# Kernel tuning notes

Hardware: AMD Instinct MI355X
Metric: run time of the kernel (lower is better)

## Reference

```python
import jax, jax.numpy as jnp
import numpy as np

L, B, D = 512, 16, 256
H = 4            # MAX_DIFF == num_heads
MAX_BONDS = 6
MAX_DIFF = 4
PROB_SHIFT = 0.3


def _attn_weights(x, Wqk, Wq, bq, Wk, bk, mask):
    """Per-head softmax(QK^T/sqrt(hd)) with key padding mask.
    x: [b,l,d]; Wqk: [d,2d] (the inc/dec_qk pre-projection);
    Wq/Wk: [d,d] (MHA in_proj, stored x@W layout); mask: [b,l] bool (True=masked).
    Returns [b,h,l,l]. The V path / out_proj of the torch MHA are discarded
    by the original module, so they are omitted here.
    """
    b, l, d = x.shape
    hd = d // H
    q = x @ Wqk[:, :d]
    k = x @ Wqk[:, d:]
    Q = (q @ Wq + bq).reshape(b, l, H, hd)
    K = (k @ Wk + bk).reshape(b, l, H, hd)
    scores = jnp.einsum('blhd,bmhd->bhlm', Q, K) / np.sqrt(hd)
    scores = jnp.where(mask[:, None, None, :], -jnp.inf, scores)
    return jax.nn.softmax(scores, axis=-1)


def setup_inputs() -> dict:
    key = jax.random.key(0)
    ks = jax.random.split(key, 16)
    s = 0.05
    p = lambda k, shape: jax.random.normal(k, shape, jnp.float32) * s
    # key_padding_mask: last 64 positions padded (True == masked)
    src_mask = jnp.broadcast_to(jnp.arange(L)[None, :] >= (L - 64), (B, L))
    return {
        'molecule_embedding': jax.random.normal(ks[0], (L, B, D), jnp.float32),
        'src_bond': jax.random.randint(ks[1], (B, L, MAX_BONDS), 0, L, jnp.int32),
        'src_mask': src_mask,
        'W_inc_qk': p(ks[2], (D, 2 * D)),
        'Wq_inc': p(ks[3], (D, D)), 'bq_inc': p(ks[4], (D,)),
        'Wk_inc': p(ks[5], (D, D)), 'bk_inc': p(ks[6], (D,)),
        'W_dec_qk': p(ks[7], (D, 2 * D)),
        'Wq_dec': p(ks[8], (D, D)), 'bq_dec': p(ks[9], (D,)),
        'Wk_dec': p(ks[10], (D, D)), 'bk_dec': p(ks[11], (D,)),
        'Wc': p(ks[12], (MAX_DIFF, MAX_DIFF)), 'bc': p(ks[13], (MAX_DIFF,)),
    }


def reference(molecule_embedding, src_bond, src_mask,
              W_inc_qk, Wq_inc, bq_inc, Wk_inc, bk_inc,
              W_dec_qk, Wq_dec, bq_dec, Wk_dec, bk_dec,
              Wc, bc):
    x = jnp.transpose(molecule_embedding, (1, 0, 2))  # [b,l,d]
    b, l, _ = x.shape

    inc = _attn_weights(x, W_inc_qk, Wq_inc, bq_inc, Wk_inc, bk_inc, src_mask)
    dec = _attn_weights(x, W_dec_qk, Wq_dec, bq_dec, Wk_dec, bk_dec, src_mask)

    pad = (~src_mask).astype(jnp.float32)              # 1 - mask
    pm2 = pad[:, :, None] * pad[:, None, :]            # [b,l,l]

    # cls_layer((inc-dec).permute(0,2,3,1)) * (MAX_DIFF*pad_mask)[...,None]
    diff = (jnp.einsum('bhlm,hc->blmc', inc - dec, Wc) + bc)
    diff = diff * (MAX_DIFF * pm2)[..., None]          # [b,l,l,4]

    # src_bond has last dim == MAX_BONDS -> one-hot neighbor counts
    src_w = jax.nn.one_hot(src_bond, l, dtype=jnp.float32).sum(axis=2) * pm2  # [b,l,l]
    eye = jnp.eye(l, dtype=jnp.float32)
    src_w = src_w * (1.0 - eye)[None]                  # zero diagonal

    # _shift_probs(src_weight.long(), prob_shift, MAX_DIFF)
    oh = jax.nn.one_hot(src_w.astype(jnp.int32), MAX_DIFF, dtype=jnp.float32)
    probs = oh * (1.0 - PROB_SHIFT) + (1.0 - oh) * (PROB_SHIFT / (MAX_DIFF - 1))
    probs = probs / probs.sum(axis=-1, keepdims=True)

    return jnp.log(probs + 1e-6) + diff                # [b,l,l,4]
```

## Files before the change

kernel.cpp:

```cpp
#include <hip/hip_runtime.h>
#include <stdint.h>

typedef unsigned short u16t;
typedef short s8v __attribute__((ext_vector_type(8)));
typedef float f4v __attribute__((ext_vector_type(4)));

#define MFMA16 __builtin_amdgcn_mfma_f32_16x16x32_bf16
#define QKN (16*4*512*64)

__device__ __forceinline__ u16t f2bf(float f) {
  unsigned u = __builtin_bit_cast(unsigned, f);
  u += 0x7fffu + ((u >> 16) & 1u);
  return (u16t)(u >> 16);
}

__global__ __launch_bounds__(256) void prep_kernel(
    const float* __restrict__ Wiqk, const float* __restrict__ Wqi, const float* __restrict__ Wki,
    const float* __restrict__ Wdqk, const float* __restrict__ Wqd, const float* __restrict__ Wkd,
    u16t* __restrict__ weffT, const int* __restrict__ mraw, int* __restrict__ mdst) {
  __shared__ float At[16][65];
  __shared__ float Bt[16][65];
  __shared__ int mode;
  const int tid = threadIdx.x;

  if (blockIdx.z == 4) {
    if (tid == 0) mode = 0;
    __syncthreads();
    unsigned v0 = (unsigned)mraw[tid], v1 = (unsigned)mraw[tid + 256];
    if (v0 == 0x3F800000u || v1 == 0x3F800000u) mode = 2;
    __syncthreads();
    if (mode == 0 && (v0 > 1u || v1 > 1u)) mode = 1;
    __syncthreads();
    const int g = blockIdx.y * 4 + blockIdx.x;
#pragma unroll
    for (int i = 0; i < 2; ++i) {
      int idx = g * 512 + i * 256 + tid;
      int m;
      if (mode == 2)      m = (((const float*)mraw)[idx] != 0.0f) ? 1 : 0;
      else if (mode == 1) m = ((const unsigned char*)mraw)[idx];
      else                m = mraw[idx];
      mdst[idx] = m;
    }
    return;
  }

  const int n0 = blockIdx.x * 64;
  const int d0 = blockIdx.y * 64;
  const int p  = blockIdx.z;
  const float* A2  = (p == 0) ? Wqi : (p == 1) ? Wki : (p == 2) ? Wqd : Wkd;
  const float* Wqk = (p < 2) ? Wiqk : Wdqk;
  const int aoff = (p & 1) * 256;
  const int tx = tid & 15, ty = tid >> 4;

  float acc[4][4];
#pragma unroll
  for (int i = 0; i < 4; ++i)
#pragma unroll
    for (int j = 0; j < 4; ++j) acc[i][j] = 0.f;

  for (int k0 = 0; k0 < 256; k0 += 16) {
    __syncthreads();
    {
      int nn = tid & 63, kr = tid >> 6;
#pragma unroll
      for (int pass = 0; pass < 4; ++pass) {
        int kk = kr + pass * 4;
        At[kk][nn] = A2[(size_t)(k0 + kk) * 256 + n0 + nn];
      }
      int kk = tid & 15, dr = tid >> 4;
#pragma unroll
      for (int pass = 0; pass < 4; ++pass) {
        int dd = dr + pass * 16;
        Bt[kk][dd] = Wqk[(size_t)(d0 + dd) * 512 + aoff + k0 + kk];
      }
    }
    __syncthreads();
#pragma unroll
    for (int kk = 0; kk < 16; ++kk) {
      float a[4], b[4];
#pragma unroll
      for (int i = 0; i < 4; ++i) a[i] = At[kk][ty * 4 + i];
#pragma unroll
      for (int j = 0; j < 4; ++j) b[j] = Bt[kk][tx * 4 + j];
#pragma unroll
      for (int i = 0; i < 4; ++i)
#pragma unroll
        for (int j = 0; j < 4; ++j) acc[i][j] = fmaf(a[i], b[j], acc[i][j]);
    }
  }

#pragma unroll
  for (int i = 0; i < 4; ++i) {
    u16t h[4] = {f2bf(acc[i][0]), f2bf(acc[i][1]), f2bf(acc[i][2]), f2bf(acc[i][3])};
    *(uint2*)(&weffT[((size_t)(p * 256 + n0 + ty * 4 + i)) * 256 + d0 + tx * 4]) =
        *(const uint2*)h;
  }
}

__global__ __launch_bounds__(256) void proj_kernel(
    const float* __restrict__ emb, const u16t* __restrict__ weffT,
    const float* __restrict__ bq_inc, const float* __restrict__ bk_inc,
    const float* __restrict__ bq_dec, const float* __restrict__ bk_dec,
    u16t* __restrict__ qk) {
  __shared__ __align__(16) u16t As[128 * 40];
  __shared__ __align__(16) u16t Bs[128 * 40];
  const int t = threadIdx.x;
  const int f = (int)(blockIdx.x + gridDim.x * blockIdx.y);
  const int xcd = f & 7, idx = f >> 3;
  const int ry = xcd * 8 + (idx & 7);
  const int nx = idx >> 3;
  const int n0 = nx * 128;
  const int r0 = ry * 128;
  const int bb = r0 >> 9;
  const int l0 = r0 & 511;
  const int lane = t & 63, wid = t >> 6;
  const int quad = lane >> 4, c15 = lane & 15;
  const int wm = wid >> 1, wn = wid & 1;

  f4v acc[4][4];
#pragma unroll
  for (int i = 0; i < 4; ++i)
#pragma unroll
    for (int j = 0; j < 4; ++j) acc[i][j] = f4v{0.f, 0.f, 0.f, 0.f};

  for (int k0 = 0; k0 < 256; k0 += 32) {
    __syncthreads();
#pragma unroll
    for (int i = 0; i < 2; ++i) {
      int c = t + i * 256;
      int m = c >> 2, off = (c & 3) * 8;
      const float* src = emb + (size_t)((l0 + m) * 16 + bb) * 256 + k0 + off;
      float4 x0 = *(const float4*)src;
      float4 x1 = *(const float4*)(src + 4);
      unsigned p0, p1, p2, p3;
      asm("v_cvt_pk_bf16_f32 %0, %1, %2" : "=v"(p0) : "v"(x0.x), "v"(x0.y));
      asm("v_cvt_pk_bf16_f32 %0, %1, %2" : "=v"(p1) : "v"(x0.z), "v"(x0.w));
      asm("v_cvt_pk_bf16_f32 %0, %1, %2" : "=v"(p2) : "v"(x1.x), "v"(x1.y));
      asm("v_cvt_pk_bf16_f32 %0, %1, %2" : "=v"(p3) : "v"(x1.z), "v"(x1.w));
      uint4 pk = make_uint4(p0, p1, p2, p3);
      *(uint4*)(&As[m * 40 + off]) = pk;
      *(uint4*)(&Bs[m * 40 + off]) =
          *(const uint4*)(weffT + (size_t)(n0 + m) * 256 + k0 + off);
    }
    __syncthreads();
    s8v af[4], bf[4];
#pragma unroll
    for (int mi = 0; mi < 4; ++mi)
      af[mi] = *(const s8v*)(&As[(wm * 64 + mi * 16 + c15) * 40 + quad * 8]);
#pragma unroll
    for (int ni = 0; ni < 4; ++ni)
      bf[ni] = *(const s8v*)(&Bs[(wn * 64 + ni * 16 + c15) * 40 + quad * 8]);
#pragma unroll
    for (int mi = 0; mi < 4; ++mi)
#pragma unroll
      for (int ni = 0; ni < 4; ++ni)
        acc[mi][ni] = MFMA16(af[mi], bf[ni], acc[mi][ni], 0, 0, 0);
  }

  const float* biasP[4] = {bq_inc, bk_inc, bq_dec, bk_dec};
#pragma unroll
  for (int ni = 0; ni < 4; ++ni) {
    int n = n0 + wn * 64 + ni * 16 + c15;
    int p = n >> 8, h = (n >> 6) & 3, tt = n & 63, jj = n & 255;
    float bias = biasP[p][jj];
    const float osc = (p & 1) ? 1.0f : 0.125f;
    u16t* dst = qk + (size_t)p * QKN;
#pragma unroll
    for (int mi = 0; mi < 4; ++mi) {
#pragma unroll
      for (int reg = 0; reg < 4; ++reg) {
        int l = l0 + wm * 64 + mi * 16 + quad * 4 + reg;
        dst[((size_t)(bb * 4 + h) * 512 + l) * 64 + tt] =
            f2bf((acc[mi][ni][reg] + bias) * osc);
      }
    }
  }
}

__global__ __launch_bounds__(512) void fused_kernel(
    const u16t* __restrict__ qk, const int* __restrict__ mask,
    const int* __restrict__ src_bond, const float* __restrict__ Wc,
    const float* __restrict__ bc, float* __restrict__ out) {
  __shared__ __align__(16) u16t Qs[8 * 16 * 72];
  __shared__ int bondsL[96];
  __shared__ int mlds[512 + 16];
  __shared__ __align__(16) float rpart[2][16][8];
  __shared__ float wlds[16];
  const int t = threadIdx.x;

  const int f = (int)(blockIdx.x + gridDim.x * blockIdx.y);
  const int j = f >> 3;
  const int bb = (f & 7) * 2 + (j >> 5);
  const int l0 = (j & 31) * 16;

  const int lane = t & 63, wid = t >> 6;
  const int quad = lane >> 4, c15 = lane & 15;
  const int mbase = wid * 64 + c15;
  const u16t* Kblk = qk + (size_t)(bb * 4) * 512 * 64;
  const int loff = mbase * 64 + quad * 8;

#pragma unroll
  for (int i = 0; i < 2; ++i) {
    int c = t + i * 512;
    int q = c >> 7, row = (c >> 3) & 15, off = (c & 7) * 8;
    const u16t* Qb = qk + (size_t)(2 * (q >> 2)) * QKN;
    *(uint4*)(&Qs[(q * 16 + row) * 72 + off]) =
        *(const uint4*)(Qb + ((size_t)(bb * 4 + (q & 3)) * 512 + l0 + row) * 64 + off);
  }
  mlds[t] = mask[bb * 512 + t];
  if (t < 16) mlds[512 + t] = mask[bb * 512 + l0 + t];
  if (t < 96) bondsL[t] = src_bond[(size_t)(bb * 512 + l0 + t / 6) * 6 + (t % 6)];
  if (t >= 96 && t < 112) wlds[t - 96] = Wc[t - 96];

  s8v kb0[4], kb1[4];
  {
    const u16t* Kq = Kblk + (size_t)1 * QKN;
#pragma unroll
    for (int nt = 0; nt < 4; ++nt) {
      kb0[nt] = *(const s8v*)(Kq + loff + nt * 1024);
      kb1[nt] = *(const s8v*)(Kq + loff + nt * 1024 + 32);
    }
  }

  __syncthreads();

  bool mskm[4];
#pragma unroll
  for (int nt = 0; nt < 4; ++nt) mskm[nt] = (mlds[mbase + nt * 16] != 0);

  float dacc[4][4][4];
#pragma unroll
  for (int nt = 0; nt < 4; ++nt)
#pragma unroll
    for (int r = 0; r < 4; ++r)
#pragma unroll
      for (int c = 0; c < 4; ++c) dacc[nt][r][c] = 0.f;

#pragma unroll 1
  for (int q = 0; q < 8; ++q) {
    const int h = q & 3;
    s8v a0 = *(const s8v*)(&Qs[(q * 16 + c15) * 72 + quad * 8]);
    s8v a1 = *(const s8v*)(&Qs[(q * 16 + c15) * 72 + 32 + quad * 8]);
    float wv[4];
#pragma unroll
    for (int c = 0; c < 4; ++c) wv[c] = wlds[h * 4 + c];

    f4v s[4];
#pragma unroll
    for (int nt = 0; nt < 4; ++nt) {
      f4v sacc = f4v{0.f, 0.f, 0.f, 0.f};
      sacc = MFMA16(a0, kb0[nt], sacc, 0, 0, 0);
      sacc = MFMA16(a1, kb1[nt], sacc, 0, 0, 0);
      s[nt] = sacc;
    }

    if (q < 7) {
      const int qn = q + 1;
      const u16t* Kq = Kblk + (size_t)(2 * (qn >> 2) + 1) * QKN
                            + (size_t)(qn & 3) * (512 * 64);
#pragma unroll
      for (int nt = 0; nt < 4; ++nt) {
        kb0[nt] = *(const s8v*)(Kq + loff + nt * 1024);
        kb1[nt] = *(const s8v*)(Kq + loff + nt * 1024 + 32);
      }
    }

    float E[4][4];
    float rsum[4] = {0.f, 0.f, 0.f, 0.f};
#pragma unroll
    for (int nt = 0; nt < 4; ++nt) {
#pragma unroll
      for (int reg = 0; reg < 4; ++reg) {
        float e = mskm[nt] ? 0.f : __expf(s[nt][reg]);
        E[nt][reg] = e;
        rsum[reg] += e;
      }
    }
#pragma unroll
    for (int reg = 0; reg < 4; ++reg) {
#pragma unroll
      for (int off = 1; off < 16; off <<= 1) rsum[reg] += __shfl_xor(rsum[reg], off);
    }
    if (c15 == 0) {
#pragma unroll
      for (int reg = 0; reg < 4; ++reg) rpart[q & 1][quad * 4 + reg][wid] = rsum[reg];
    }

    asm volatile("s_waitcnt lgkmcnt(0)" ::: "memory");
    __builtin_amdgcn_s_barrier();
    asm volatile("" ::: "memory");

    const float sgn = (q < 4) ? 1.f : -1.f;
    float inv[4];
#pragma unroll
    for (int reg = 0; reg < 4; ++reg) {
      const float4* rp = (const float4*)&rpart[q & 1][quad * 4 + reg][0];
      float4 s0 = rp[0], s1 = rp[1];
      float tot = s0.x + s0.y + s0.z + s0.w + s1.x + s1.y + s1.z + s1.w;
      inv[reg] = sgn * __builtin_amdgcn_rcpf(tot);
    }

#pragma unroll
    for (int nt = 0; nt < 4; ++nt) {
#pragma unroll
      for (int reg = 0; reg < 4; ++reg) {
        float P = E[nt][reg] * inv[reg];
#pragma unroll
        for (int c = 0; c < 4; ++c)
          dacc[nt][reg][c] = fmaf(P, wv[c], dacc[nt][reg][c]);
      }
    }
  }

  float bcF[4];
#pragma unroll
  for (int c = 0; c < 4; ++c) bcF[c] = bc[c];
  const float lgH = logf(0.7f + 1e-6f);
  const float lgM = logf(0.1f + 1e-6f);
  const float lgU = logf(0.25f + 1e-6f);

#pragma unroll
  for (int nt = 0; nt < 4; ++nt) {
    int m = mbase + nt * 16;
    bool padm = !mskm[nt];
#pragma unroll
    for (int reg = 0; reg < 4; ++reg) {
      int lloc = quad * 4 + reg;
      int l = l0 + lloc;
      bool padl = (mlds[512 + lloc] == 0);
      bool pm = padl && padm;
      int cnt = 0;
#pragma unroll
      for (int j6 = 0; j6 < 6; ++j6) cnt += (bondsL[lloc * 6 + j6] == m) ? 1 : 0;
      int cls = (pm && (m != l)) ? cnt : 0;
      float v[4];
#pragma unroll
      for (int c = 0; c < 4; ++c) {
        float lp = (cls >= 4) ? lgU : ((c == cls) ? lgH : lgM);
        float dv = pm ? 4.f * (dacc[nt][reg][c] + bcF[c]) : 0.f;
        v[c] = lp + dv;
      }
      float4 o = make_float4(v[0], v[1], v[2], v[3]);
      *(float4*)(&out[((size_t)(bb * 512 + l) * 512 + m) * 4]) = o;
    }
  }
}

extern "C" void kernel_launch(void* const* d_in, const int* in_sizes, int n_in,
                              void* d_out, int out_size, void* d_ws, size_t ws_size,
                              hipStream_t stream) {
  (void)in_sizes; (void)n_in; (void)out_size; (void)ws_size;
  const float* emb      = (const float*)d_in[0];
  const int*   src_bond = (const int*)d_in[1];
  const int*   mask_raw = (const int*)d_in[2];
  const float* W_inc_qk = (const float*)d_in[3];
  const float* Wq_inc   = (const float*)d_in[4];
  const float* bq_inc   = (const float*)d_in[5];
  const float* Wk_inc   = (const float*)d_in[6];
  const float* bk_inc   = (const float*)d_in[7];
  const float* W_dec_qk = (const float*)d_in[8];
  const float* Wq_dec   = (const float*)d_in[9];
  const float* bq_dec   = (const float*)d_in[10];
  const float* Wk_dec   = (const float*)d_in[11];
  const float* bk_dec   = (const float*)d_in[12];
  const float* Wc       = (const float*)d_in[13];
  const float* bc       = (const float*)d_in[14];
  float* out = (float*)d_out;

  char* ws = (char*)d_ws;
  int*   wsMask = (int*)ws;
  u16t*  weffT  = (u16t*)(ws + 32768);
  u16t*  qk     = (u16t*)(ws + 32768 + 524288);

  hipLaunchKernelGGL(prep_kernel, dim3(4, 4, 5), dim3(256), 0, stream,
                     W_inc_qk, Wq_inc, Wk_inc, W_dec_qk, Wq_dec, Wk_dec, weffT,
                     mask_raw, wsMask);
  hipLaunchKernelGGL(proj_kernel, dim3(8, 64), dim3(256), 0, stream,
                     emb, weffT, bq_inc, bk_inc, bq_dec, bk_dec, qk);
  hipLaunchKernelGGL(fused_kernel, dim3(32, 16), dim3(512), 0, stream,
                     qk, wsMask, src_bond, Wc, bc, out);
}
```

Baseline: 178.5 us.

## Software-pipeline softmax normalization fold one head behind score computation

Restructures the 8-step head loop into pairs with double-buffered exponent arrays, so each step folds the previous head's normalized probabilities into the accumulator before the barrier. The next head's MFMA score work then overlaps the reduction wait, and the rcp/FMA fold no longer sits directly after the barrier. It also raises wave priority around the MFMAs. The cost is more live registers (two E arrays) and larger unrolled code. The rpart double-buffer parity must stay consistent for the fold to read the correct sums.

New measurement: 174.7 us. 2.1% less time.

```diff
diff --git a/kernel.cpp b/kernel.cpp
--- a/kernel.cpp
+++ b/kernel.cpp
@@ -236,81 +236,97 @@
 #pragma unroll
       for (int c = 0; c < 4; ++c) dacc[nt][r][c] = 0.f;
 
+  float Ea[4][4], Eb[4][4];
+
+#define FOLD_PREV(QP, EARR, PAR)                                              \
+  {                                                                           \
+    const int hp = (QP) & 3;                                                  \
+    const float sgp = ((QP) < 4) ? 1.f : -1.f;                                \
+    float wvp[4];                                                             \
+    _Pragma("unroll")                                                         \
+    for (int c = 0; c < 4; ++c) wvp[c] = wlds[hp * 4 + c];                    \
+    float inv[4];                                                             \
+    _Pragma("unroll")                                                         \
+    for (int reg = 0; reg < 4; ++reg) {                                       \
+      const float4* rp = (const float4*)&rpart[PAR][quad * 4 + reg][0];       \
+      float4 s0 = rp[0], s1 = rp[1];                                          \
+      float tot = s0.x + s0.y + s0.z + s0.w + s1.x + s1.y + s1.z + s1.w;      \
+      inv[reg] = sgp * __builtin_amdgcn_rcpf(tot);                            \
+    }                                                                         \
+    _Pragma("unroll")                                                         \
+    for (int nt = 0; nt < 4; ++nt) {                                          \
+      _Pragma("unroll")                                                       \
+      for (int reg = 0; reg < 4; ++reg) {                                     \
+        float P = EARR[nt][reg] * inv[reg];                                   \
+        _Pragma("unroll")                                                     \
+        for (int c = 0; c < 4; ++c)                                           \
+          dacc[nt][reg][c] = fmaf(P, wvp[c], dacc[nt][reg][c]);               \
+      }                                                                       \
+    }                                                                         \
+  }
+
+#define COMBO_BODY(Q, EARR, DO_FOLD, QP, EPREV, PARP)                         \
+  {                                                                           \
+    s8v a0 = *(const s8v*)(&Qs[((Q) * 16 + c15) * 72 + quad * 8]);            \
+    s8v a1 = *(const s8v*)(&Qs[((Q) * 16 + c15) * 72 + 32 + quad * 8]);       \
+    __builtin_amdgcn_s_setprio(1);                                            \
+    f4v s[4];                                                                 \
+    _Pragma("unroll")                                                         \
+    for (int nt = 0; nt < 4; ++nt) {                                          \
+      f4v sacc = f4v{0.f, 0.f, 0.f, 0.f};                                     \
+      sacc = MFMA16(a0, kb0[nt], sacc, 0, 0, 0);                              \
+      sacc = MFMA16(a1, kb1[nt], sacc, 0, 0, 0);                              \
+      s[nt] = sacc;                                                           \
+    }                                                                         \
+    __builtin_amdgcn_s_setprio(0);                                            \
+    if ((Q) < 7) {                                                            \
+      const int qn = (Q) + 1;                                                 \
+      const u16t* Kq = Kblk + (size_t)(2 * (qn >> 2) + 1) * QKN               \
+                            + (size_t)(qn & 3) * (512 * 64);                  \
+      _Pragma("unroll")                                                       \
+      for (int nt = 0; nt < 4; ++nt) {                                        \
+        kb0[nt] = *(const s8v*)(Kq + loff + nt * 1024);                       \
+        kb1[nt] = *(const s8v*)(Kq + loff + nt * 1024 + 32);                  \
+      }                                                                       \
+    }                                                                         \
+    float rsum[4] = {0.f, 0.f, 0.f, 0.f};                                     \
+    _Pragma("unroll")                                                         \
+    for (int nt = 0; nt < 4; ++nt) {                                          \
+      _Pragma("unroll")                                                       \
+      for (int reg = 0; reg < 4; ++reg) {                                     \
+        float e = mskm[nt] ? 0.f : __expf(s[nt][reg]);                        \
+        EARR[nt][reg] = e;                                                    \
+        rsum[reg] += e;                                                       \
+      }                                                                       \
+    }                                                                         \
+    _Pragma("unroll")                                                         \
+    for (int reg = 0; reg < 4; ++reg) {                                       \
+      _Pragma("unroll")                                                       \
+      for (int off = 1; off < 16; off <<= 1)                                  \
+        rsum[reg] += __shfl_xor(rsum[reg], off);                              \
+    }                                                                         \
+    if (c15 == 0) {                                                           \
+      _Pragma("unroll")                                                       \
+      for (int reg = 0; reg < 4; ++reg)                                       \
+        rpart[(Q) & 1][quad * 4 + reg][wid] = rsum[reg];                      \
+    }                                                                         \
+    if (DO_FOLD) FOLD_PREV(QP, EPREV, PARP);                                  \
+    asm volatile("s_waitcnt lgkmcnt(0)" ::: "memory");                        \
+    __builtin_amdgcn_s_barrier();                                             \
+    asm volatile("" ::: "memory");                                            \
+  }
+
 #pragma unroll 1
-  for (int q = 0; q < 8; ++q) {
-    const int h = q & 3;
-    s8v a0 = *(const s8v*)(&Qs[(q * 16 + c15) * 72 + quad * 8]);
-    s8v a1 = *(const s8v*)(&Qs[(q * 16 + c15) * 72 + 32 + quad * 8]);
-    float wv[4];
-#pragma unroll
-    for (int c = 0; c < 4; ++c) wv[c] = wlds[h * 4 + c];
-
-    f4v s[4];
-#pragma unroll
-    for (int nt = 0; nt < 4; ++nt) {
-      f4v sacc = f4v{0.f, 0.f, 0.f, 0.f};
-      sacc = MFMA16(a0, kb0[nt], sacc, 0, 0, 0);
-      sacc = MFMA16(a1, kb1[nt], sacc, 0, 0, 0);
-      s[nt] = sacc;
-    }
-
-    if (q < 7) {
-      const int qn = q + 1;
-      const u16t* Kq = Kblk + (size_t)(2 * (qn >> 2) + 1) * QKN
-                            + (size_t)(qn & 3) * (512 * 64);
-#pragma unroll
-      for (int nt = 0; nt < 4; ++nt) {
-        kb0[nt] = *(const s8v*)(Kq + loff + nt * 1024);
-        kb1[nt] = *(const s8v*)(Kq + loff + nt * 1024 + 32);
-      }
-    }
-
-    float E[4][4];
-    float rsum[4] = {0.f, 0.f, 0.f, 0.f};
-#pragma unroll
-    for (int nt = 0; nt < 4; ++nt) {
-#pragma unroll
-      for (int reg = 0; reg < 4; ++reg) {
-        float e = mskm[nt] ? 0.f : __expf(s[nt][reg]);
-        E[nt][reg] = e;
-        rsum[reg] += e;
-      }
-    }
-#pragma unroll
-    for (int reg = 0; reg < 4; ++reg) {
-#pragma unroll
-      for (int off = 1; off < 16; off <<= 1) rsum[reg] += __shfl_xor(rsum[reg], off);
-    }
-    if (c15 == 0) {
-#pragma unroll
-      for (int reg = 0; reg < 4; ++reg) rpart[q & 1][quad * 4 + reg][wid] = rsum[reg];
-    }
-
-    asm volatile("s_waitcnt lgkmcnt(0)" ::: "memory");
-    __builtin_amdgcn_s_barrier();
-    asm volatile("" ::: "memory");
-
-    const float sgn = (q < 4) ? 1.f : -1.f;
-    float inv[4];
-#pragma unroll
-    for (int reg = 0; reg < 4; ++reg) {
-      const float4* rp = (const float4*)&rpart[q & 1][quad * 4 + reg][0];
-      float4 s0 = rp[0], s1 = rp[1];
-      float tot = s0.x + s0.y + s0.z + s0.w + s1.x + s1.y + s1.z + s1.w;
-      inv[reg] = sgn * __builtin_amdgcn_rcpf(tot);
-    }
-
-#pragma unroll
-    for (int nt = 0; nt < 4; ++nt) {
-#pragma unroll
-      for (int reg = 0; reg < 4; ++reg) {
-        float P = E[nt][reg] * inv[reg];
-#pragma unroll
-        for (int c = 0; c < 4; ++c)
-          dacc[nt][reg][c] = fmaf(P, wv[c], dacc[nt][reg][c]);
-      }
-    }
-  }
+  for (int qq = 0; qq < 4; ++qq) {
+    const int q0 = 2 * qq;
+    COMBO_BODY(q0, Ea, (qq > 0), (q0 - 1), Eb, 1);
+    const int q1 = 2 * qq + 1;
+    COMBO_BODY(q1, Eb, 1, q0, Ea, 0);
+  }
+  FOLD_PREV(7, Eb, 1);
+
+#undef COMBO_BODY
+#undef FOLD_PREV
 
   float bcF[4];
 #pragma unroll
```

## Process two heads per iteration, halve barriers, use DPP row reductions

Applied to the files above, without the earlier changes.

The softmax loop now handles two head slices per iteration, so the workgroup barrier for cross-wave row-sum exchange runs four times instead of eight. The 16-lane row-sum reduction uses DPP row-shift adds instead of shuffle xor. The explicit software prefetch of the next K block into registers is dropped in favour of loading K directly inside each iteration. This cuts synchronisation and shuffle cost but raises register pressure and may expose global-load latency.

After: 182.5 us. 2.3% more time.

```diff
diff --git a/kernel.cpp b/kernel.cpp
--- a/kernel.cpp
+++ b/kernel.cpp
@@ -12,6 +12,19 @@
   unsigned u = __builtin_bit_cast(unsigned, f);
   u += 0x7fffu + ((u >> 16) & 1u);
   return (u16t)(u >> 16);
+}
+
+__device__ __forceinline__ float rowred16(float x) {
+  int t;
+  t = __builtin_amdgcn_update_dpp(0, __builtin_bit_cast(int, x), 0x128, 0xf, 0xf, false);
+  x += __builtin_bit_cast(float, t);
+  t = __builtin_amdgcn_update_dpp(0, __builtin_bit_cast(int, x), 0x124, 0xf, 0xf, false);
+  x += __builtin_bit_cast(float, t);
+  t = __builtin_amdgcn_update_dpp(0, __builtin_bit_cast(int, x), 0x122, 0xf, 0xf, false);
+  x += __builtin_bit_cast(float, t);
+  t = __builtin_amdgcn_update_dpp(0, __builtin_bit_cast(int, x), 0x121, 0xf, 0xf, false);
+  x += __builtin_bit_cast(float, t);
+  return x;
 }
 
 __global__ __launch_bounds__(256) void prep_kernel(
@@ -184,7 +197,7 @@
   __shared__ __align__(16) u16t Qs[8 * 16 * 72];
   __shared__ int bondsL[96];
   __shared__ int mlds[512 + 16];
-  __shared__ __align__(16) float rpart[2][16][8];
+  __shared__ __align__(16) float rpart[2][2][16][8];
   __shared__ float wlds[16];
   const int t = threadIdx.x;
 
@@ -212,102 +225,112 @@
   if (t < 96) bondsL[t] = src_bond[(size_t)(bb * 512 + l0 + t / 6) * 6 + (t % 6)];
   if (t >= 96 && t < 112) wlds[t - 96] = Wc[t - 96];
 
-  s8v kb0[4], kb1[4];
-  {
-    const u16t* Kq = Kblk + (size_t)1 * QKN;
+  __syncthreads();
+
+  bool mskm[4];
+#pragma unroll
+  for (int nt = 0; nt < 4; ++nt) mskm[nt] = (mlds[mbase + nt * 16] != 0);
+
+  float dacc[4][4][4];
+#pragma unroll
+  for (int nt = 0; nt < 4; ++nt)
+#pragma unroll
+    for (int r = 0; r < 4; ++r)
+#pragma unroll
+      for (int c = 0; c < 4; ++c) dacc[nt][r][c] = 0.f;
+
+#pragma unroll 1
+  for (int r = 0; r < 4; ++r) {
+    const int qa = 2 * r, qb = 2 * r + 1;
+    const int ha = qa & 3, hb = qb & 3;
+    const float sgn = (r < 2) ? 1.f : -1.f;
+
+    const u16t* Ka = Kblk + (size_t)(2 * (qa >> 2) + 1) * QKN
+                          + (size_t)(qa & 3) * (512 * 64);
+    s8v aa0 = *(const s8v*)(&Qs[(qa * 16 + c15) * 72 + quad * 8]);
+    s8v aa1 = *(const s8v*)(&Qs[(qa * 16 + c15) * 72 + 32 + quad * 8]);
+    f4v sa[4];
 #pragma unroll
     for (int nt = 0; nt < 4; ++nt) {
-      kb0[nt] = *(const s8v*)(Kq + loff + nt * 1024);
-      kb1[nt] = *(const s8v*)(Kq + loff + nt * 1024 + 32);
-    }
-  }
-
-  __syncthreads();
-
-  bool mskm[4];
-#pragma unroll
-  for (int nt = 0; nt < 4; ++nt) mskm[nt] = (mlds[mbase + nt * 16] != 0);
-
-  float dacc[4][4][4];
-#pragma unroll
-  for (int nt = 0; nt < 4; ++nt)
-#pragma unroll
-    for (int r = 0; r < 4; ++r)
-#pragma unroll
-      for (int c = 0; c < 4; ++c) dacc[nt][r][c] = 0.f;
-
-#pragma unroll 1
-  for (int q = 0; q < 8; ++q) {
-    const int h = q & 3;
-    s8v a0 = *(const s8v*)(&Qs[(q * 16 + c15) * 72 + quad * 8]);
-    s8v a1 = *(const s8v*)(&Qs[(q * 16 + c15) * 72 + 32 + quad * 8]);
-    float wv[4];
-#pragma unroll
-    for (int c = 0; c < 4; ++c) wv[c] = wlds[h * 4 + c];
-
-    f4v s[4];
+      s8v k0 = *(const s8v*)(Ka + loff + nt * 1024);
+      s8v k1 = *(const s8v*)(Ka + loff + nt * 1024 + 32);
+      f4v sacc = f4v{0.f, 0.f, 0.f, 0.f};
+      sacc = MFMA16(aa0, k0, sacc, 0, 0, 0);
+      sacc = MFMA16(aa1, k1, sacc, 0, 0, 0);
+      sa[nt] = sacc;
+    }
+
+    const u16t* Kb = Kblk + (size_t)(2 * (qb >> 2) + 1) * QKN
+                          + (size_t)(qb & 3) * (512 * 64);
+    s8v ab0 = *(const s8v*)(&Qs[(qb * 16 + c15) * 72 + quad * 8]);
+    s8v ab1 = *(const s8v*)(&Qs[(qb * 16 + c15) * 72 + 32 + quad * 8]);
+    f4v sb[4];
 #pragma unroll
     for (int nt = 0; nt < 4; ++nt) {
+      s8v k0 = *(const s8v*)(Kb + loff + nt * 1024);
+      s8v k1 = *(const s8v*)(Kb + loff + nt * 1024 + 32);
       f4v sacc = f4v{0.f, 0.f, 0.f, 0.f};
-      sacc = MFMA16(a0, kb0[nt], sacc, 0, 0, 0);
-      sacc = MFMA16(a1, kb1[nt], sacc, 0, 0, 0);
-      s[nt] = sacc;
-    }
-
-    if (q < 7) {
-      const int qn = q + 1;
-      const u16t* Kq = Kblk + (size_t)(2 * (qn >> 2) + 1) * QKN
-                            + (size_t)(qn & 3) * (512 * 64);
-#pragma unroll
-      for (int nt = 0; nt < 4; ++nt) {
-        kb0[nt] = *(const s8v*)(Kq + loff + nt * 1024);
-        kb1[nt] = *(const s8v*)(Kq + loff + nt * 1024 + 32);
-      }
-    }
-
-    float E[4][4];
-    float rsum[4] = {0.f, 0.f, 0.f, 0.f};
+      sacc = MFMA16(ab0, k0, sacc, 0, 0, 0);
+      sacc = MFMA16(ab1, k1, sacc, 0, 0, 0);
+      sb[nt] = sacc;
+    }
+
+    float Ea[4][4], Eb[4][4];
+    float ra[4] = {0.f, 0.f, 0.f, 0.f}, rb[4] = {0.f, 0.f, 0.f, 0.f};
 #pragma unroll
     for (int nt = 0; nt < 4; ++nt) {
 #pragma unroll
       for (int reg = 0; reg < 4; ++reg) {
-        float e = mskm[nt] ? 0.f : __expf(s[nt][reg]);
-        E[nt][reg] = e;
-        rsum[reg] += e;
+        float ea = mskm[nt] ? 0.f : __expf(sa[nt][reg]);
+        float eb = mskm[nt] ? 0.f : __expf(sb[nt][reg]);
+        Ea[nt][reg] = ea;  ra[reg] += ea;
+        Eb[nt][reg] = eb;  rb[reg] += eb;
       }
     }
 #pragma unroll
     for (int reg = 0; reg < 4; ++reg) {
-#pragma unroll
-      for (int off = 1; off < 16; off <<= 1) rsum[reg] += __shfl_xor(rsum[reg], off);
+      ra[reg] = rowred16(ra[reg]);
+      rb[reg] = rowred16(rb[reg]);
     }
     if (c15 == 0) {
 #pragma unroll
-      for (int reg = 0; reg < 4; ++reg) rpart[q & 1][quad * 4 + reg][wid] = rsum[reg];
+      for (int reg = 0; reg < 4; ++reg) {
+        rpart[r & 1][0][quad * 4 + reg][wid] = ra[reg];
+        rpart[r & 1][1][quad * 4 + reg][wid] = rb[reg];
+      }
     }
 
     asm volatile("s_waitcnt lgkmcnt(0)" ::: "memory");
     __builtin_amdgcn_s_barrier();
     asm volatile("" ::: "memory");
 
-    const float sgn = (q < 4) ? 1.f : -1.f;
-    float inv[4];
+    float inva[4], invb[4];
 #pragma unroll
     for (int reg = 0; reg < 4; ++reg) {
-      const float4* rp = (const float4*)&rpart[q & 1][quad * 4 + reg][0];
-      float4 s0 = rp[0], s1 = rp[1];
-      float tot = s0.x + s0.y + s0.z + s0.w + s1.x + s1.y + s1.z + s1.w;
-      inv[reg] = sgn * __builtin_amdgcn_rcpf(tot);
-    }
+      const float4* pa = (const float4*)&rpart[r & 1][0][quad * 4 + reg][0];
+      float4 a0 = pa[0], a1 = pa[1];
+      inva[reg] = sgn * __builtin_amdgcn_rcpf(
+          a0.x + a0.y + a0.z + a0.w + a1.x + a1.y + a1.z + a1.w);
+      const float4* pb = (const float4*)&rpart[r & 1][1][quad * 4 + reg][0];
+      float4 b0 = pb[0], b1 = pb[1];
+      invb[reg] = sgn * __builtin_amdgcn_rcpf(
+          b0.x + b0.y + b0.z + b0.w + b1.x + b1.y + b1.z + b1.w);
+    }
+    float wva[4], wvb[4];
+#pragma unroll
+    for (int c = 0; c < 4; ++c) { wva[c] = wlds[ha * 4 + c]; wvb[c] = wlds[hb * 4 + c]; }
 
 #pragma unroll
     for (int nt = 0; nt < 4; ++nt) {
 #pragma unroll
       for (int reg = 0; reg < 4; ++reg) {
-        float P = E[nt][reg] * inv[reg];
-#pragma unroll
-        for (int c = 0; c < 4; ++c)
-          dacc[nt][reg][c] = fmaf(P, wv[c], dacc[nt][reg][c]);
+        float Pa = Ea[nt][reg] * inva[reg];
+        float Pb = Eb[nt][reg] * invb[reg];
+#pragma unroll
+        for (int c = 0; c < 4; ++c) {
+          float d = fmaf(Pa, wva[c], dacc[nt][reg][c]);
+          dacc[nt][reg][c] = fmaf(Pb, wvb[c], d);
+        }
       }
     }
   }
```

## Pre-convert embeddings to bf16 once and skip fully masked attention tiles

Applied to the files above, without the earlier changes.

A new group of prep-kernel blocks converts the fp32 embedding to bf16 once into workspace. The projection kernel then loads bf16 directly instead of converting fp32 on every tile, halving the A-operand global read per tile, though the extra pass costs an fp32 read plus a bf16 write. The fused kernel also skips the whole head loop when every query row in its block is padded, and skips MFMA, exp and accumulation for warps whose key columns are all masked. The barrier is kept so synchronisation stays uniform.

New measurement: 172.8 us. 1.03x faster.

```diff
diff --git a/kernel.cpp b/kernel.cpp
--- a/kernel.cpp
+++ b/kernel.cpp
@@ -17,11 +17,29 @@
 __global__ __launch_bounds__(256) void prep_kernel(
     const float* __restrict__ Wiqk, const float* __restrict__ Wqi, const float* __restrict__ Wki,
     const float* __restrict__ Wdqk, const float* __restrict__ Wqd, const float* __restrict__ Wkd,
-    u16t* __restrict__ weffT, const int* __restrict__ mraw, int* __restrict__ mdst) {
+    u16t* __restrict__ weffT, const int* __restrict__ mraw, int* __restrict__ mdst,
+    const float* __restrict__ emb, u16t* __restrict__ embh) {
   __shared__ float At[16][65];
   __shared__ float Bt[16][65];
   __shared__ int mode;
   const int tid = threadIdx.x;
+
+  if (blockIdx.z >= 5) {
+    const int g2 = (blockIdx.z - 5) * 16 + blockIdx.y * 4 + blockIdx.x;
+#pragma unroll
+    for (int it = 0; it < 8; ++it) {
+      size_t idx = (size_t)g2 * 16384 + it * 2048 + tid * 8;
+      float4 x0 = *(const float4*)(emb + idx);
+      float4 x1 = *(const float4*)(emb + idx + 4);
+      unsigned p0, p1, p2, p3;
+      asm("v_cvt_pk_bf16_f32 %0, %1, %2" : "=v"(p0) : "v"(x0.x), "v"(x0.y));
+      asm("v_cvt_pk_bf16_f32 %0, %1, %2" : "=v"(p1) : "v"(x0.z), "v"(x0.w));
+      asm("v_cvt_pk_bf16_f32 %0, %1, %2" : "=v"(p2) : "v"(x1.x), "v"(x1.y));
+      asm("v_cvt_pk_bf16_f32 %0, %1, %2" : "=v"(p3) : "v"(x1.z), "v"(x1.w));
+      *(uint4*)(embh + idx) = make_uint4(p0, p1, p2, p3);
+    }
+    return;
+  }
 
   if (blockIdx.z == 4) {
     if (tid == 0) mode = 0;
@@ -98,7 +116,7 @@
 }
 
 __global__ __launch_bounds__(256) void proj_kernel(
-    const float* __restrict__ emb, const u16t* __restrict__ weffT,
+    const u16t* __restrict__ embh, const u16t* __restrict__ weffT,
     const float* __restrict__ bq_inc, const float* __restrict__ bk_inc,
     const float* __restrict__ bq_dec, const float* __restrict__ bk_dec,
     u16t* __restrict__ qk) {
@@ -129,16 +147,8 @@
     for (int i = 0; i < 2; ++i) {
       int c = t + i * 256;
       int m = c >> 2, off = (c & 3) * 8;
-      const float* src = emb + (size_t)((l0 + m) * 16 + bb) * 256 + k0 + off;
-      float4 x0 = *(const float4*)src;
-      float4 x1 = *(const float4*)(src + 4);
-      unsigned p0, p1, p2, p3;
-      asm("v_cvt_pk_bf16_f32 %0, %1, %2" : "=v"(p0) : "v"(x0.x), "v"(x0.y));
-      asm("v_cvt_pk_bf16_f32 %0, %1, %2" : "=v"(p1) : "v"(x0.z), "v"(x0.w));
-      asm("v_cvt_pk_bf16_f32 %0, %1, %2" : "=v"(p2) : "v"(x1.x), "v"(x1.y));
-      asm("v_cvt_pk_bf16_f32 %0, %1, %2" : "=v"(p3) : "v"(x1.z), "v"(x1.w));
-      uint4 pk = make_uint4(p0, p1, p2, p3);
-      *(uint4*)(&As[m * 40 + off]) = pk;
+      *(uint4*)(&As[m * 40 + off]) =
+          *(const uint4*)(embh + (size_t)((l0 + m) * 16 + bb) * 256 + k0 + off);
       *(uint4*)(&Bs[m * 40 + off]) =
           *(const uint4*)(weffT + (size_t)(n0 + m) * 256 + k0 + off);
     }
@@ -227,6 +237,10 @@
   bool mskm[4];
 #pragma unroll
   for (int nt = 0; nt < 4; ++nt) mskm[nt] = (mlds[mbase + nt * 16] != 0);
+  const bool allm = mskm[0] && mskm[1] && mskm[2] && mskm[3];
+  bool lskip = true;
+#pragma unroll
+  for (int i = 0; i < 16; ++i) lskip = lskip && (mlds[512 + i] != 0);
 
   float dacc[4][4][4];
 #pragma unroll
@@ -236,78 +250,90 @@
 #pragma unroll
       for (int c = 0; c < 4; ++c) dacc[nt][r][c] = 0.f;
 
+  if (!lskip) {
 #pragma unroll 1
-  for (int q = 0; q < 8; ++q) {
-    const int h = q & 3;
-    s8v a0 = *(const s8v*)(&Qs[(q * 16 + c15) * 72 + quad * 8]);
-    s8v a1 = *(const s8v*)(&Qs[(q * 16 + c15) * 72 + 32 + quad * 8]);
-    float wv[4];
-#pragma unroll
-    for (int c = 0; c < 4; ++c) wv[c] = wlds[h * 4 + c];
-
-    f4v s[4];
-#pragma unroll
-    for (int nt = 0; nt < 4; ++nt) {
-      f4v sacc = f4v{0.f, 0.f, 0.f, 0.f};
-      sacc = MFMA16(a0, kb0[nt], sacc, 0, 0, 0);
-      sacc = MFMA16(a1, kb1[nt], sacc, 0, 0, 0);
-      s[nt] = sacc;
-    }
-
-    if (q < 7) {
-      const int qn = q + 1;
-      const u16t* Kq = Kblk + (size_t)(2 * (qn >> 2) + 1) * QKN
-                            + (size_t)(qn & 3) * (512 * 64);
-#pragma unroll
-      for (int nt = 0; nt < 4; ++nt) {
-        kb0[nt] = *(const s8v*)(Kq + loff + nt * 1024);
-        kb1[nt] = *(const s8v*)(Kq + loff + nt * 1024 + 32);
-      }
-    }
-
-    float E[4][4];
-    float rsum[4] = {0.f, 0.f, 0.f, 0.f};
-#pragma unroll
-    for (int nt = 0; nt < 4; ++nt) {
-#pragma unroll
-      for (int reg = 0; reg < 4; ++reg) {
-        float e = mskm[nt] ? 0.f : __expf(s[nt][reg]);
-        E[nt][reg] = e;
-        rsum[reg] += e;
-      }
-    }
-#pragma unroll
-    for (int reg = 0; reg < 4; ++reg) {
-#pragma unroll
-      for (int off = 1; off < 16; off <<= 1) rsum[reg] += __shfl_xor(rsum[reg], off);
-    }
-    if (c15 == 0) {
-#pragma unroll
-      for (int reg = 0; reg < 4; ++reg) rpart[q & 1][quad * 4 + reg][wid] = rsum[reg];
-    }
-
-    asm volatile("s_waitcnt lgkmcnt(0)" ::: "memory");
-    __builtin_amdgcn_s_barrier();
-    asm volatile("" ::: "memory");
-
-    const float sgn = (q < 4) ? 1.f : -1.f;
-    float inv[4];
-#pragma unroll
-    for (int reg = 0; reg < 4; ++reg) {
-      const float4* rp = (const float4*)&rpart[q & 1][quad * 4 + reg][0];
-      float4 s0 = rp[0], s1 = rp[1];
-      float tot = s0.x + s0.y + s0.z + s0.w + s1.x + s1.y + s1.z + s1.w;
-      inv[reg] = sgn * __builtin_amdgcn_rcpf(tot);
-    }
-
-#pragma unroll
-    for (int nt = 0; nt < 4; ++nt) {
-#pragma unroll
-      for (int reg = 0; reg < 4; ++reg) {
-        float P = E[nt][reg] * inv[reg];
-#pragma unroll
-        for (int c = 0; c < 4; ++c)
-          dacc[nt][reg][c] = fmaf(P, wv[c], dacc[nt][reg][c]);
+    for (int q = 0; q < 8; ++q) {
+      const int h = q & 3;
+      s8v a0 = *(const s8v*)(&Qs[(q * 16 + c15) * 72 + quad * 8]);
+      s8v a1 = *(const s8v*)(&Qs[(q * 16 + c15) * 72 + 32 + quad * 8]);
+      float wv[4];
+#pragma unroll
+      for (int c = 0; c < 4; ++c) wv[c] = wlds[h * 4 + c];
+
+      float E[4][4];
+      float rsum[4] = {0.f, 0.f, 0.f, 0.f};
+      if (!allm) {
+        f4v s[4];
+#pragma unroll
+        for (int nt = 0; nt < 4; ++nt) {
+          f4v sacc = f4v{0.f, 0.f, 0.f, 0.f};
+          sacc = MFMA16(a0, kb0[nt], sacc, 0, 0, 0);
+          sacc = MFMA16(a1, kb1[nt], sacc, 0, 0, 0);
+          s[nt] = sacc;
+        }
+
+        if (q < 7) {
+          const int qn = q + 1;
+          const u16t* Kq = Kblk + (size_t)(2 * (qn >> 2) + 1) * QKN
+                                + (size_t)(qn & 3) * (512 * 64);
+#pragma unroll
+          for (int nt = 0; nt < 4; ++nt) {
+            kb0[nt] = *(const s8v*)(Kq + loff + nt * 1024);
+            kb1[nt] = *(const s8v*)(Kq + loff + nt * 1024 + 32);
+          }
+        }
+
+#pragma unroll
+        for (int nt = 0; nt < 4; ++nt) {
+#pragma unroll
+          for (int reg = 0; reg < 4; ++reg) {
+            float e = mskm[nt] ? 0.f : __expf(s[nt][reg]);
+            E[nt][reg] = e;
+            rsum[reg] += e;
+          }
+        }
+#pragma unroll
+        for (int reg = 0; reg < 4; ++reg) {
+#pragma unroll
+          for (int off = 1; off < 16; off <<= 1)
+            rsum[reg] += __shfl_xor(rsum[reg], off);
+        }
+      } else {
+#pragma unroll
+        for (int nt = 0; nt < 4; ++nt)
+#pragma unroll
+          for (int reg = 0; reg < 4; ++reg) E[nt][reg] = 0.f;
+      }
+      if (c15 == 0) {
+#pragma unroll
+        for (int reg = 0; reg < 4; ++reg)
+          rpart[q & 1][quad * 4 + reg][wid] = rsum[reg];
+      }
+
+      asm volatile("s_waitcnt lgkmcnt(0)" ::: "memory");
+      __builtin_amdgcn_s_barrier();
+      asm volatile("" ::: "memory");
+
+      if (!allm) {
+        const float sgn = (q < 4) ? 1.f : -1.f;
+        float inv[4];
+#pragma unroll
+        for (int reg = 0; reg < 4; ++reg) {
+          const float4* rp = (const float4*)&rpart[q & 1][quad * 4 + reg][0];
+          float4 s0 = rp[0], s1 = rp[1];
+          float tot = s0.x + s0.y + s0.z + s0.w + s1.x + s1.y + s1.z + s1.w;
+          inv[reg] = sgn * __builtin_amdgcn_rcpf(tot);
+        }
+#pragma unroll
+        for (int nt = 0; nt < 4; ++nt) {
+#pragma unroll
+          for (int reg = 0; reg < 4; ++reg) {
+            float P = E[nt][reg] * inv[reg];
+#pragma unroll
+            for (int c = 0; c < 4; ++c)
+              dacc[nt][reg][c] = fmaf(P, wv[c], dacc[nt][reg][c]);
+          }
+        }
       }
     }
   }
@@ -371,12 +397,13 @@
   int*   wsMask = (int*)ws;
   u16t*  weffT  = (u16t*)(ws + 32768);
   u16t*  qk     = (u16t*)(ws + 32768 + 524288);
-
-  hipLaunchKernelGGL(prep_kernel, dim3(4, 4, 5), dim3(256), 0, stream,
+  u16t*  embh   = (u16t*)(ws + 32768 + 524288 + 16777216);
+
+  hipLaunchKernelGGL(prep_kernel, dim3(4, 4, 13), dim3(256), 0, stream,
                      W_inc_qk, Wq_inc, Wk_inc, W_dec_qk, Wq_dec, Wk_dec, weffT,
-                     mask_raw, wsMask);
+                     mask_raw, wsMask, emb, embh);
   hipLaunchKernelGGL(proj_kernel, dim3(8, 64), dim3(256), 0, stream,
-                     emb, weffT, bq_inc, bk_inc, bq_dec, bk_dec, qk);
+                     embh, weffT, bq_inc, bk_inc, bq_dec, bk_dec, qk);
   hipLaunchKernelGGL(fused_kernel, dim3(32, 16), dim3(512), 0, stream,
                      qk, wsMask, src_bond, Wc, bc, out);
 }
```
